# Kernel tuning notes

Measured on AMD Instinct MI355X. Metric: run time of the kernel, lower is better.

Reference implementation:

```python
import jax, jax.numpy as jnp
import numpy as np

D = 1024      # embedding_dim
H = 16        # num_heads
DH = D // H   # head_dim
DFF = 4 * D
EPS = 1e-5


def setup_inputs() -> dict:
    key = jax.random.key(0)
    ks = jax.random.split(key, 10)
    B, T = 2, 2048
    s = 0.02
    return {
        "x": jax.random.normal(ks[0], (B, T, D), dtype=jnp.float32),
        "Wq": jax.random.normal(ks[1], (H, D, DH), dtype=jnp.float32) * s,
        "Wk": jax.random.normal(ks[2], (H, D, DH), dtype=jnp.float32) * s,
        "Wv": jax.random.normal(ks[3], (H, D, DH), dtype=jnp.float32) * s,
        "W1": jax.random.normal(ks[4], (D, DFF), dtype=jnp.float32) * s,
        "b1": jnp.zeros((DFF,), dtype=jnp.float32),
        "W2": jax.random.normal(ks[5], (DFF, D), dtype=jnp.float32) * s,
        "b2": jnp.zeros((D,), dtype=jnp.float32),
        "gamma1": jnp.ones((D,), dtype=jnp.float32),
        "beta1": jnp.zeros((D,), dtype=jnp.float32),
        "gamma2": jnp.ones((D,), dtype=jnp.float32),
        "beta2": jnp.zeros((D,), dtype=jnp.float32),
    }


def _layernorm(x, gamma, beta):
    # torch.var default is unbiased (ddof=1) -- faithful to LayerNorm1d
    mean = jnp.mean(x, axis=-1, keepdims=True)
    var = jnp.var(x, axis=-1, keepdims=True, ddof=1)
    return gamma * (x - mean) * jax.lax.rsqrt(var + EPS) + beta


def _block(x, Wq, Wk, Wv, W1, b1, W2, b2, gamma1, beta1, gamma2, beta2):
    B, T, _ = x.shape
    h = _layernorm(x, gamma1, beta1)
    # per-head projections stacked: [B,H,T,DH]
    Q = jnp.einsum('btd,hde->bhte', h, Wq)
    K = jnp.einsum('btd,hde->bhte', h, Wk)
    V = jnp.einsum('btd,hde->bhte', h, Wv)
    # NOTE: original scales by 1/sqrt(embedding_dim), NOT head_dim
    scores = jnp.einsum('bhqe,bhke->bhqk', Q, K) / jnp.sqrt(jnp.float32(D))
    causal = jnp.tril(jnp.ones((T, T), dtype=bool))
    scores = jnp.where(causal, scores, -jnp.inf)
    attn = jax.nn.softmax(scores, axis=-1)
    out = jnp.einsum('bhqk,bhke->bhqe', attn, V)
    # torch.cat over heads along last dim == transpose+reshape
    out = out.transpose(0, 2, 1, 3).reshape(B, T, D)
    x = x + out
    h2 = _layernorm(x, gamma2, beta2)
    ff = jax.nn.relu(h2 @ W1 + b1) @ W2 + b2  # dropout is identity at inference
    return x + ff


def reference(x, Wq, Wk, Wv, W1, b1, W2, b2, gamma1, beta1, gamma2, beta2):
    return _block(x, Wq, Wk, Wv, W1, b1, W2, b2, gamma1, beta1, gamma2, beta2)
```

## Files before the change

kernel.cpp:

```cpp
#include <hip/hip_runtime.h>

typedef unsigned short u16;
typedef __bf16 bf16;
typedef __attribute__((ext_vector_type(8))) __bf16 bf16x8;
typedef __attribute__((ext_vector_type(4))) float f32x4;
typedef __attribute__((ext_vector_type(8))) unsigned short u16x8;
typedef unsigned long long u64;

__device__ __forceinline__ float bf2f(u16 h) {
  return __uint_as_float(((unsigned int)h) << 16);
}
__device__ __forceinline__ u16 f2bf(float f) {
  unsigned int u = __float_as_uint(f);
  return (u16)((u + 0x7fffu + ((u >> 16) & 1u)) >> 16);
}
__device__ __forceinline__ u16 ld_cv(const void* p, size_t i, int f32) {
  return f32 ? f2bf(((const float*)p)[i]) : ((const u16*)p)[i];
}
__device__ __forceinline__ float ld_f(const void* p, size_t i, int f32) {
  return f32 ? ((const float*)p)[i] : bf2f(((const u16*)p)[i]);
}
__device__ __forceinline__ void async16(const u16* g, u16* l) {
  __builtin_amdgcn_global_load_lds(
      (const __attribute__((address_space(1))) unsigned int*)g,
      (__attribute__((address_space(3))) unsigned int*)l, 16, 0, 0);
}
__device__ __forceinline__ unsigned pk_bf16(float hi, float lo) {
  return __builtin_amdgcn_perm(__float_as_uint(hi) + 0x8000u,
                               __float_as_uint(lo) + 0x8000u, 0x07060302u);
}

__global__ void sniff_kernel(const u16* __restrict__ x, int* __restrict__ flag) {
  const int tid = threadIdx.x;
  int me = 0;
#pragma unroll
  for (int j = 0; j < 4; j++) {
    const u16 v = x[(tid * 4 + j) * 2];
    const int e = (v >> 7) & 0xFF;
    me = me > e ? me : e;
  }
#pragma unroll
  for (int off = 32; off > 0; off >>= 1) {
    const int o = __shfl_down(me, off);
    me = me > o ? me : o;
  }
  __shared__ int sm[4];
  if ((tid & 63) == 0) sm[tid >> 6] = me;
  __syncthreads();
  if (tid == 0) {
    int a = sm[0] > sm[1] ? sm[0] : sm[1];
    int b = sm[2] > sm[3] ? sm[2] : sm[3];
    *flag = ((a > b ? a : b) >= 140) ? 1 : 0;
  }
}

__global__ void prep_kernel(const void* __restrict__ Wq, const void* __restrict__ Wk,
                            const void* __restrict__ Wv, const void* __restrict__ W1,
                            const void* __restrict__ W2,
                            u16* __restrict__ WTq, u16* __restrict__ W1T,
                            u16* __restrict__ W2T, const int* __restrict__ flag) {
  __shared__ u16 tile[64][65];
  const int f = *flag;
  const int bid = blockIdx.x;
  const int lx = threadIdx.x & 63, ly = threadIdx.x >> 6;
  if (bid < 768) {
    const int bx = bid & 15, wh = bid >> 4;
    const int w = wh >> 4, hh = wh & 15;
    const int tr = bx * 64;
    const void* W = (w == 0) ? Wq : ((w == 1) ? Wk : Wv);
    const size_t hbase = (size_t)hh * 65536;
#pragma unroll
    for (int i = 0; i < 16; i++)
      tile[ly * 16 + i][lx] = ld_cv(W, hbase + (size_t)(tr + ly * 16 + i) * 64 + lx, f);
    __syncthreads();
#pragma unroll
    for (int i = 0; i < 16; i++)
      WTq[((size_t)(w * 1024 + hh * 64 + ly * 16 + i)) * 1024 + tr + lx] =
          tile[lx][ly * 16 + i];
  } else {
    const void* src;
    u16* dst;
    int R, C, tc, tr;
    if (bid < 1792) {
      const int j = bid - 768;
      src = W1; dst = W1T; R = 1024; C = 4096;
      tc = (j & 63) * 64; tr = (j >> 6) * 64;
    } else {
      const int j = bid - 1792;
      src = W2; dst = W2T; R = 4096; C = 1024;
      tc = (j & 15) * 64; tr = (j >> 4) * 64;
    }
#pragma unroll
    for (int i = 0; i < 16; i++)
      tile[ly * 16 + i][lx] = ld_cv(src, (size_t)(tr + ly * 16 + i) * C + tc + lx, f);
    __syncthreads();
#pragma unroll
    for (int i = 0; i < 16; i++)
      dst[(size_t)(tc + ly * 16 + i) * R + tr + lx] = tile[lx][ly * 16 + i];
  }
}

template <int EPI, int WR, int WC, bool MS>
__launch_bounds__(WR * WC * 64)
__global__ void gemm_bt(const u16* __restrict__ A, const u16* __restrict__ B,
                        int K, int KLD, int NX, int N,
                        const void* __restrict__ bias, const u16* __restrict__ res,
                        void* __restrict__ out,
                        u16* __restrict__ Qo, u16* __restrict__ Ko, u16* __restrict__ Vto,
                        const int* __restrict__ flag) {
  constexpr int BM = WR * 64, BN = WC * 64, T = WR * WC * 64;
  constexpr int RPA = T / 4;
  constexpr int RAH = BM / RPA;
  constexpr int RBH = BN / RPA;
  __shared__ __align__(16) u16 As[BM * 64];
  __shared__ __align__(16) u16 Bs[BN * 64];
  const int tid = threadIdx.x;
  const int bid = blockIdx.x;
  const int sxp = NX >> 3;
  const int xcd = bid & 7, j9 = bid >> 3;
  int m0, n0, koff = 0, khb = 0;
  if (EPI == 3) {
    m0 = (xcd * 4 + (j9 & 3)) * BM;
    n0 = ((j9 >> 2) & 7) * BN;
    khb = (j9 >> 5) & 1;
    koff = khb * K;
  } else if (MS) {
    m0 = (xcd * sxp + j9 % sxp) * BM;
    n0 = (j9 / sxp) * BN;
  } else {
    n0 = (xcd * sxp + j9 % sxp) * BN;
    m0 = (j9 / sxp) * BM;
  }
  const int wave = tid >> 6, lane = tid & 63;
  const int wm = (wave / WC) * 64, wn = (wave % WC) * 64;
  const int lm = lane & 15, lq = lane >> 4;
  const int fb = (EPI == 1 || EPI == 2) ? *flag : 0;

  const f32x4 zero = {0.f, 0.f, 0.f, 0.f};
  f32x4 acc[4][4];
#pragma unroll
  for (int i = 0; i < 4; i++)
#pragma unroll
    for (int j = 0; j < 4; j++) acc[i][j] = zero;

  const int ar = tid >> 2;
  const int ac = ((tid & 3) ^ ((tid >> 3) & 3)) * 8;
  const u16* Ag = A + (size_t)(m0 + ar) * KLD + koff + ac;
  const u16* Bg = B + (size_t)(n0 + ar) * KLD + koff + ac;
  u16* AsP = &As[tid * 8];
  u16* BsP = &Bs[tid * 8];
  const int rq = (lq ^ ((lm >> 1) & 3)) * 8;

  for (int k0 = 0; k0 < K; k0 += 64) {
#pragma unroll
    for (int hh = 0; hh < 2; hh++) {
#pragma unroll
      for (int c = 0; c < RAH; c++)
        async16(Ag + k0 + hh * 32 + (size_t)c * RPA * KLD,
                AsP + hh * BM * 32 + c * RPA * 32);
#pragma unroll
      for (int c = 0; c < RBH; c++)
        async16(Bg + k0 + hh * 32 + (size_t)c * RPA * KLD,
                BsP + hh * BN * 32 + c * RPA * 32);
    }
    __syncthreads();
    bf16x8 a0[4], a1[4], b0[4], b1[4];
#pragma unroll
    for (int i = 0; i < 4; i++) {
      a0[i] = *(const bf16x8*)&As[(wm + i * 16 + lm) * 32 + rq];
      a1[i] = *(const bf16x8*)&As[BM * 32 + (wm + i * 16 + lm) * 32 + rq];
    }
#pragma unroll
    for (int i = 0; i < 4; i++) {
      b0[i] = *(const bf16x8*)&Bs[(wn + i * 16 + lm) * 32 + rq];
      b1[i] = *(const bf16x8*)&Bs[BN * 32 + (wn + i * 16 + lm) * 32 + rq];
    }
#pragma unroll
    for (int i = 0; i < 4; i++)
#pragma unroll
      for (int j = 0; j < 4; j++) {
        acc[i][j] = __builtin_amdgcn_mfma_f32_16x16x32_bf16(a0[i], b0[j], acc[i][j], 0, 0, 0);
        acc[i][j] = __builtin_amdgcn_mfma_f32_16x16x32_bf16(a1[i], b1[j], acc[i][j], 0, 0, 0);
      }
    __syncthreads();
  }

  if (EPI == 0) {
#pragma unroll
    for (int i = 0; i < 4; i++) {
      const int row0 = m0 + wm + i * 16 + lq * 4;
      const int bb = row0 >> 11, t0 = row0 & 2047;
#pragma unroll
      for (int j = 0; j < 4; j++) {
        const int col = n0 + wn + j * 16 + lm;
        const int w = col >> 10, nn = col & 1023;
        const int hh = nn >> 6, e = nn & 63;
        if (w == 2) {
          ushort4 v4;
          v4.x = f2bf(acc[i][j][0]);
          v4.y = f2bf(acc[i][j][1]);
          v4.z = f2bf(acc[i][j][2]);
          v4.w = f2bf(acc[i][j][3]);
          *(ushort4*)&Vto[(((size_t)(bb * 16 + hh)) * 64 + e) * 2048 + t0] = v4;
        } else {
          u16* dst = (w == 0) ? Qo : Ko;
#pragma unroll
          for (int r = 0; r < 4; r++)
            dst[(((size_t)(bb * 16 + hh)) * 2048 + t0 + r) * 64 + e] =
                f2bf(acc[i][j][r]);
        }
      }
    }
  } else if (EPI == 3) {
    u16* P = khb ? Ko : Qo;
#pragma unroll
    for (int i = 0; i < 4; i++) {
#pragma unroll
      for (int r = 0; r < 4; r++) {
        const int row = m0 + wm + i * 16 + lq * 4 + r;
#pragma unroll
        for (int j = 0; j < 4; j++) {
          const int col = n0 + wn + j * 16 + lm;
          P[(size_t)row * N + col] = f2bf(acc[i][j][r]);
        }
      }
    }
  } else {
#pragma unroll
    for (int i = 0; i < 4; i++) {
#pragma unroll
      for (int r = 0; r < 4; r++) {
        const int row = m0 + wm + i * 16 + lq * 4 + r;
#pragma unroll
        for (int j = 0; j < 4; j++) {
          const int col = n0 + wn + j * 16 + lm;
          const float c = acc[i][j][r];
          if (EPI == 1) {
            const float v = c + ld_f(bias, col, fb);
            ((u16*)out)[(size_t)row * N + col] = f2bf(v > 0.f ? v : 0.f);
          } else {
            const float v = c + ld_f(bias, col, fb) + bf2f(res[(size_t)row * N + col]);
            if (fb)
              ((float*)out)[(size_t)row * N + col] = v;
            else
              ((u16*)out)[(size_t)row * N + col] = f2bf(v);
          }
        }
      }
    }
  }
}

__launch_bounds__(256)
__global__ void ffn2_reduce(const u16* __restrict__ P0, const u16* __restrict__ P1,
                            const void* __restrict__ bias, const u16* __restrict__ res,
                            void* __restrict__ out, const int* __restrict__ flag) {
  const int f = *flag;
  const size_t i0 = ((size_t)blockIdx.x * 256 + threadIdx.x) * 8;
  const int col = (int)(i0 & 1023);
  const u16x8 a8 = *(const u16x8*)(P0 + i0);
  const u16x8 b8 = *(const u16x8*)(P1 + i0);
  const u16x8 r8 = *(const u16x8*)(res + i0);
  float v[8];
#pragma unroll
  for (int k = 0; k < 8; k++)
    v[k] = bf2f(a8[k]) + bf2f(b8[k]) + ld_f(bias, col + k, f) + bf2f(r8[k]);
  if (f) {
    float4 o0 = {v[0], v[1], v[2], v[3]};
    float4 o1 = {v[4], v[5], v[6], v[7]};
    *(float4*)((float*)out + i0) = o0;
    *(float4*)((float*)out + i0 + 4) = o1;
  } else {
    u16x8 o8;
#pragma unroll
    for (int k = 0; k < 8; k++) o8[k] = f2bf(v[k]);
    *(u16x8*)((u16*)out + i0) = o8;
  }
}

__launch_bounds__(256)
__global__ void attn_mfma(const u16* __restrict__ Q, const u16* __restrict__ K,
                          const u16* __restrict__ Vt, const void* __restrict__ xres,
                          const int* __restrict__ flag, u16* __restrict__ x2) {
  __shared__ __align__(16) unsigned char smem[66048];
  const int tid = threadIdx.x;
  const int wave = tid >> 6, lane = tid & 63;
  const int lm = lane & 15, quad = lane >> 4;
  const int bid = blockIdx.x;
  const int xcd = bid & 7, jj = bid >> 3;
  const int bh = xcd + 8 * (jj & 3);
  const int pair = jj >> 2;
  const int b = bh >> 4, h = bh & 15;
  const int f32in = *flag;

  u16* stw = (u16*)smem + wave * 8192;
  float (*Olds)[32][68] = (float(*)[32][68])smem;
  float (*Llds)[2][16] = (float(*)[2][16])(smem + 65536);

  const u16* Kbh = K + (size_t)bh * 131072;
  const u16* Vbh = Vt + (size_t)bh * 131072;
  const f32x4 zero = {0.f, 0.f, 0.f, 0.f};
  const int srow = lane >> 2;
  const int sch2 = ((lane & 3) ^ ((srow >> 1) & 3)) * 8;
  const int rk = (lm >> 1) & 3;

  union V8 { bf16x8 v; struct { u64 lo, hi; } q; };

  auto stageKV = [&](int t, u16* buf) {
    const int ks = t * 32;
#pragma unroll
    for (int hh2 = 0; hh2 < 2; hh2++)
#pragma unroll
      for (int c = 0; c < 2; c++)
        async16(Kbh + (size_t)(ks + c * 16 + srow) * 64 + hh2 * 32 + sch2,
                buf + hh2 * 1024 + c * 512 + lane * 8);
#pragma unroll
    for (int c = 0; c < 4; c++)
      async16(Vbh + (size_t)(c * 16 + srow) * 2048 + ks + sch2,
              buf + 2048 + c * 512 + lane * 8);
  };

#pragma unroll 1
  for (int phase = 0; phase < 2; phase++) {
    const int qb = phase ? (63 - pair) : pair;
    const int qw0 = qb * 32;

    bf16x8 qf[2][2];
#pragma unroll
    for (int s = 0; s < 2; s++) {
      const u16* Qp = Q + ((size_t)bh * 2048 + qw0 + s * 16 + lm) * 64 + quad * 8;
      qf[s][0] = *(const bf16x8*)Qp;
      qf[s][1] = *(const bf16x8*)(Qp + 32);
    }
    f32x4 ot[2][4];
#pragma unroll
    for (int s = 0; s < 2; s++)
#pragma unroll
      for (int j = 0; j < 4; j++) ot[s][j] = zero;
    float l[2] = {0.f, 0.f};

    const int nt = qb + 1;
    const int si = (nt * wave) >> 2;
    const int ei = (nt * (wave + 1)) >> 2;

    if (si < ei) stageKV(si, stw);

#pragma unroll 1
    for (int t = si; t < ei; t++) {
      const u16* Ksw = stw + ((t - si) & 1) * 4096;
      const u16* Vsw = Ksw + 2048;
      if (t + 1 < ei) {
        stageKV(t + 1, stw + ((t - si + 1) & 1) * 4096);
        asm volatile("s_waitcnt vmcnt(8)" ::: "memory");
      } else {
        asm volatile("s_waitcnt vmcnt(0)" ::: "memory");
      }

      f32x4 S[2][2];
      __builtin_amdgcn_s_setprio(1);
#pragma unroll
      for (int s = 0; s < 2; s++)
#pragma unroll
        for (int hh = 0; hh < 2; hh++) {
          const bf16x8 k0 =
              *(const bf16x8*)&Ksw[(hh * 16 + lm) * 32 + (quad ^ rk) * 8];
          const bf16x8 k1 =
              *(const bf16x8*)&Ksw[1024 + (hh * 16 + lm) * 32 + (quad ^ rk) * 8];
          f32x4 a = zero;
          a = __builtin_amdgcn_mfma_f32_16x16x32_bf16(k0, qf[s][0], a, 0, 0, 0);
          a = __builtin_amdgcn_mfma_f32_16x16x32_bf16(k1, qf[s][1], a, 0, 0, 0);
          S[s][hh] = a;
        }
      __builtin_amdgcn_s_setprio(0);

      const bool maskT = (t == qb);
#pragma unroll
      for (int s = 0; s < 2; s++) {
        float p[2][4];
#pragma unroll
        for (int hh = 0; hh < 2; hh++)
#pragma unroll
          for (int r = 0; r < 4; r++)
            p[hh][r] = __expf(S[s][hh][r] * 0.03125f);
        if (maskT) {
#pragma unroll
          for (int hh = 0; hh < 2; hh++)
#pragma unroll
            for (int r = 0; r < 4; r++)
              if (hh * 16 + quad * 4 + r > s * 16 + lm) p[hh][r] = 0.f;
        }
#pragma unroll
        for (int hh = 0; hh < 2; hh++)
#pragma unroll
          for (int r = 0; r < 4; r++) l[s] += p[hh][r];
        unsigned pk[4];
        pk[0] = pk_bf16(p[0][1], p[0][0]);
        pk[1] = pk_bf16(p[0][3], p[0][2]);
        pk[2] = pk_bf16(p[1][1], p[1][0]);
        pk[3] = pk_bf16(p[1][3], p[1][2]);
        const bf16x8 pf = *(const bf16x8*)pk;
        __builtin_amdgcn_s_setprio(1);
#pragma unroll
        for (int j = 0; j < 4; j++) {
          V8 vf;
          vf.q.lo = *(const u64*)&Vsw[(j * 16 + lm) * 32 +
                                      (((quad >> 1)) ^ rk) * 8 + (quad & 1) * 4];
          vf.q.hi = *(const u64*)&Vsw[(j * 16 + lm) * 32 +
                                      (((quad >> 1) | 2) ^ rk) * 8 + (quad & 1) * 4];
          ot[s][j] = __builtin_amdgcn_mfma_f32_16x16x32_bf16(vf.v, pf, ot[s][j], 0, 0, 0);
        }
        __builtin_amdgcn_s_setprio(0);
      }
    }

#pragma unroll
    for (int s = 0; s < 2; s++) {
      l[s] += __shfl_xor(l[s], 16);
      l[s] += __shfl_xor(l[s], 32);
    }

    __syncthreads();

#pragma unroll
    for (int s = 0; s < 2; s++)
#pragma unroll
      for (int j = 0; j < 4; j++)
        *(f32x4*)&Olds[wave][s * 16 + lm][j * 16 + quad * 4] = ot[s][j];
    if (quad == 0) {
      Llds[wave][0][lm] = l[0];
      Llds[wave][1][lm] = l[1];
    }
    __syncthreads();
    const int q = tid >> 3;
    const int e0 = (tid & 7) * 8;
    f32x4 oa = zero, ob = zero;
#pragma unroll
    for (int w = 0; w < 4; w++) {
      oa += *(const f32x4*)&Olds[w][q][e0];
      ob += *(const f32x4*)&Olds[w][q][e0 + 4];
    }
    const float lt = Llds[0][q >> 4][q & 15] + Llds[1][q >> 4][q & 15] +
                     Llds[2][q >> 4][q & 15] + Llds[3][q >> 4][q & 15];
    const float linv = 1.f / lt;
    const size_t rowbase = ((size_t)(b * 2048 + qw0 + q)) * 1024 + h * 64 + e0;
    float xv[8];
    if (f32in) {
      const float* xf = (const float*)xres + rowbase;
      const float4 u0 = *(const float4*)xf;
      const float4 u1 = *(const float4*)(xf + 4);
      xv[0] = u0.x; xv[1] = u0.y; xv[2] = u0.z; xv[3] = u0.w;
      xv[4] = u1.x; xv[5] = u1.y; xv[6] = u1.z; xv[7] = u1.w;
    } else {
      const u16x8 u = *(const u16x8*)((const u16*)xres + rowbase);
#pragma unroll
      for (int k = 0; k < 8; k++) xv[k] = bf2f(u[k]);
    }
    u16x8 o8;
#pragma unroll
    for (int k = 0; k < 4; k++) o8[k] = f2bf(xv[k] + oa[k] * linv);
#pragma unroll
    for (int k = 0; k < 4; k++) o8[4 + k] = f2bf(xv[4 + k] + ob[k] * linv);
    *(u16x8*)&x2[rowbase] = o8;
    __syncthreads();
  }
}

__launch_bounds__(256)
__global__ void ln_kernel(const void* __restrict__ x, const void* __restrict__ gamma,
                          const void* __restrict__ beta, u16* __restrict__ out,
                          const int* __restrict__ flag, int xraw) {
  const size_t row = blockIdx.x;
  const int tid = threadIdx.x;
  const int f = *flag;
  const int fx = xraw ? f : 0;
  float v0, v1, v2, v3;
  if (fx) {
    const float4 v = *((const float4*)x + row * 256 + tid);
    v0 = v.x; v1 = v.y; v2 = v.z; v3 = v.w;
  } else {
    const ushort4 u = *((const ushort4*)x + row * 256 + tid);
    v0 = bf2f(u.x); v1 = bf2f(u.y); v2 = bf2f(u.z); v3 = bf2f(u.w);
  }
  float s = v0 + v1 + v2 + v3;
  float sq = v0 * v0 + v1 * v1 + v2 * v2 + v3 * v3;
#pragma unroll
  for (int off = 32; off > 0; off >>= 1) {
    s += __shfl_down(s, off);
    sq += __shfl_down(sq, off);
  }
  __shared__ float ss[4], ssq[4];
  if ((tid & 63) == 0) { ss[tid >> 6] = s; ssq[tid >> 6] = sq; }
  __syncthreads();
  s = ss[0] + ss[1] + ss[2] + ss[3];
  sq = ssq[0] + ssq[1] + ssq[2] + ssq[3];
  const float mean = s * (1.f / 1024.f);
  const float var = (sq - 1024.f * mean * mean) * (1.f / 1023.f);
  const float rs = rsqrtf(var + 1e-5f);
  const int c0 = tid * 4;
  ushort4 o;
  o.x = f2bf(ld_f(gamma, c0 + 0, f) * (v0 - mean) * rs + ld_f(beta, c0 + 0, f));
  o.y = f2bf(ld_f(gamma, c0 + 1, f) * (v1 - mean) * rs + ld_f(beta, c0 + 1, f));
  o.z = f2bf(ld_f(gamma, c0 + 2, f) * (v2 - mean) * rs + ld_f(beta, c0 + 2, f));
  o.w = f2bf(ld_f(gamma, c0 + 3, f) * (v3 - mean) * rs + ld_f(beta, c0 + 3, f));
  *(ushort4*)&out[row * 1024 + tid * 4] = o;
}

extern "C" void kernel_launch(void* const* d_in, const int* in_sizes, int n_in,
                              void* d_out, int out_size, void* d_ws, size_t ws_size,
                              hipStream_t stream) {
  const void* x      = d_in[0];
  const void* Wq     = d_in[1];
  const void* Wk     = d_in[2];
  const void* Wv     = d_in[3];
  const void* W1     = d_in[4];
  const void* b1     = d_in[5];
  const void* W2     = d_in[6];
  const void* b2     = d_in[7];
  const void* gamma1 = d_in[8];
  const void* beta1  = d_in[9];
  const void* gamma2 = d_in[10];
  const void* beta2  = d_in[11];
  u16* ws = (u16*)d_ws;

  const size_t M4 = 4194304;
  u16* h   = ws;
  u16* Qb  = ws + 1 * M4;
  u16* Kb  = ws + 2 * M4;
  u16* Vtb = ws + 3 * M4;
  u16* WTq = ws + 4 * M4;
  u16* x2  = ws + 4 * M4;
  u16* h2  = ws + 5 * M4;
  u16* W1T = ws + 6 * M4;
  u16* W2T = ws + 7 * M4;
  u16* ff1 = ws;
  u16* P0  = ws + 5 * M4;
  u16* P1  = ws + 6 * M4;
  int* flag = (int*)(ws + 8 * M4 + 9216);

  sniff_kernel<<<1, 256, 0, stream>>>((const u16*)x, flag);
  prep_kernel<<<2816, 256, 0, stream>>>(Wq, Wk, Wv, W1, W2, WTq, W1T, W2T, flag);
  ln_kernel<<<4096, 256, 0, stream>>>(x, gamma1, beta1, h, flag, 1);
  gemm_bt<0, 4, 2, false><<<384, 512, 0, stream>>>(h, WTq, 1024, 1024, 24, 3072,
                                                   nullptr, nullptr, nullptr,
                                                   Qb, Kb, Vtb, flag);
  attn_mfma<<<1024, 256, 0, stream>>>(Qb, Kb, Vtb, x, flag, x2);
  ln_kernel<<<4096, 256, 0, stream>>>(x2, gamma2, beta2, h2, flag, 0);
  gemm_bt<1, 4, 2, false><<<512, 512, 0, stream>>>(h2, W1T, 1024, 1024, 32, 4096,
                                                   b1, nullptr, ff1,
                                                   nullptr, nullptr, nullptr, flag);
  gemm_bt<3, 2, 2, false><<<512, 256, 0, stream>>>(ff1, W2T, 2048, 4096, 8, 1024,
                                                   nullptr, nullptr, nullptr,
                                                   P0, P1, nullptr, flag);
  ffn2_reduce<<<2048, 256, 0, stream>>>(P0, P1, b2, x2, d_out, flag);
}
```

Measured before the change: 325.2 us.

## Restructure attention so each wave owns a query block sharing cooperatively staged K/V

The attention kernel switches from splitting the KV range of one query block across four waves (with an LDS reduction of partial outputs and row sums) to giving each wave its own 32-row query block. Two early and two late blocks share one block so causal work balances. K/V tiles are staged cooperatively by all waves into a shared double buffer with barriers, and LDS shrinks from about 66 KB to 16 KB with launch bounds allowing two blocks per CU. This removes the cross-wave reduction and the phase loop but adds per-tile block barriers and idle waves once their causal range ends. The grid is halved to 512 blocks.

```diff
diff --git a/kernel.cpp b/kernel.cpp
--- a/kernel.cpp
+++ b/kernel.cpp
@@ -278,24 +278,22 @@
   }
 }
 
-__launch_bounds__(256)
+__launch_bounds__(256, 2)
 __global__ void attn_mfma(const u16* __restrict__ Q, const u16* __restrict__ K,
                           const u16* __restrict__ Vt, const void* __restrict__ xres,
                           const int* __restrict__ flag, u16* __restrict__ x2) {
-  __shared__ __align__(16) unsigned char smem[66048];
+  __shared__ __align__(16) u16 smem[2][4096];
   const int tid = threadIdx.x;
   const int wave = tid >> 6, lane = tid & 63;
   const int lm = lane & 15, quad = lane >> 4;
   const int bid = blockIdx.x;
-  const int xcd = bid & 7, jj = bid >> 3;
-  const int bh = xcd + 8 * (jj & 3);
-  const int pair = jj >> 2;
+  const int bh = (bid & 7) + 8 * ((bid >> 3) & 3);
+  const int p = bid >> 5;
   const int b = bh >> 4, h = bh & 15;
   const int f32in = *flag;
-
-  u16* stw = (u16*)smem + wave * 8192;
-  float (*Olds)[32][68] = (float(*)[32][68])smem;
-  float (*Llds)[2][16] = (float(*)[2][16])(smem + 65536);
+  const int qb = (wave < 2) ? (2 * p + wave) : (63 - 2 * p - (wave & 1));
+  const int qw0 = qb * 32;
+  const int nt = 64 - 2 * p;
 
   const u16* Kbh = K + (size_t)bh * 131072;
   const u16* Vbh = Vt + (size_t)bh * 131072;
@@ -304,164 +302,136 @@
   const int sch2 = ((lane & 3) ^ ((srow >> 1) & 3)) * 8;
   const int rk = (lm >> 1) & 3;
 
+  bf16x8 qf[2][2];
+#pragma unroll
+  for (int s = 0; s < 2; s++) {
+    const u16* Qp = Q + ((size_t)bh * 2048 + qw0 + s * 16 + lm) * 64 + quad * 8;
+    qf[s][0] = *(const bf16x8*)Qp;
+    qf[s][1] = *(const bf16x8*)(Qp + 32);
+  }
+  __builtin_amdgcn_s_waitcnt(0x0F70);
+
+  f32x4 ot[2][4];
+#pragma unroll
+  for (int s = 0; s < 2; s++)
+#pragma unroll
+    for (int j = 0; j < 4; j++) ot[s][j] = zero;
+  float l[2] = {0.f, 0.f};
+
   union V8 { bf16x8 v; struct { u64 lo, hi; } q; };
 
-  auto stageKV = [&](int t, u16* buf) {
+  auto stage2 = [&](int t, u16* buf) {
     const int ks = t * 32;
-#pragma unroll
-    for (int hh2 = 0; hh2 < 2; hh2++)
+    if (wave < 2) {
 #pragma unroll
       for (int c = 0; c < 2; c++)
-        async16(Kbh + (size_t)(ks + c * 16 + srow) * 64 + hh2 * 32 + sch2,
-                buf + hh2 * 1024 + c * 512 + lane * 8);
-#pragma unroll
-    for (int c = 0; c < 4; c++)
-      async16(Vbh + (size_t)(c * 16 + srow) * 2048 + ks + sch2,
-              buf + 2048 + c * 512 + lane * 8);
+        async16(Kbh + (size_t)(ks + c * 16 + srow) * 64 + wave * 32 + sch2,
+                buf + wave * 1024 + c * 512 + lane * 8);
+    } else {
+      const int cb = (wave & 1) * 2;
+#pragma unroll
+      for (int c = cb; c < cb + 2; c++)
+        async16(Vbh + (size_t)(c * 16 + srow) * 2048 + ks + sch2,
+                buf + 2048 + c * 512 + lane * 8);
+    }
   };
 
+  stage2(0, smem[0]);
+
 #pragma unroll 1
-  for (int phase = 0; phase < 2; phase++) {
-    const int qb = phase ? (63 - pair) : pair;
-    const int qw0 = qb * 32;
-
-    bf16x8 qf[2][2];
-#pragma unroll
-    for (int s = 0; s < 2; s++) {
-      const u16* Qp = Q + ((size_t)bh * 2048 + qw0 + s * 16 + lm) * 64 + quad * 8;
-      qf[s][0] = *(const bf16x8*)Qp;
-      qf[s][1] = *(const bf16x8*)(Qp + 32);
-    }
-    f32x4 ot[2][4];
-#pragma unroll
-    for (int s = 0; s < 2; s++)
-#pragma unroll
-      for (int j = 0; j < 4; j++) ot[s][j] = zero;
-    float l[2] = {0.f, 0.f};
-
-    const int nt = qb + 1;
-    const int si = (nt * wave) >> 2;
-    const int ei = (nt * (wave + 1)) >> 2;
-
-    if (si < ei) stageKV(si, stw);
-
-#pragma unroll 1
-    for (int t = si; t < ei; t++) {
-      const u16* Ksw = stw + ((t - si) & 1) * 4096;
+  for (int t = 0; t < nt; t++) {
+    if (t + 1 < nt) {
+      stage2(t + 1, smem[(t + 1) & 1]);
+      asm volatile("s_waitcnt vmcnt(2)" ::: "memory");
+    } else {
+      asm volatile("s_waitcnt vmcnt(0)" ::: "memory");
+    }
+    __builtin_amdgcn_s_barrier();
+    if (t <= qb) {
+      const u16* Ksw = smem[t & 1];
       const u16* Vsw = Ksw + 2048;
-      if (t + 1 < ei) {
-        stageKV(t + 1, stw + ((t - si + 1) & 1) * 4096);
-        asm volatile("s_waitcnt vmcnt(8)" ::: "memory");
-      } else {
-        asm volatile("s_waitcnt vmcnt(0)" ::: "memory");
-      }
-
+      bf16x8 kk[2][2];
+#pragma unroll
+      for (int hh = 0; hh < 2; hh++) {
+        kk[hh][0] = *(const bf16x8*)&Ksw[(hh * 16 + lm) * 32 + (quad ^ rk) * 8];
+        kk[hh][1] = *(const bf16x8*)&Ksw[1024 + (hh * 16 + lm) * 32 + (quad ^ rk) * 8];
+      }
+      V8 vf[4];
+#pragma unroll
+      for (int j = 0; j < 4; j++) {
+        vf[j].q.lo = *(const u64*)&Vsw[(j * 16 + lm) * 32 +
+                                       (((quad >> 1)) ^ rk) * 8 + (quad & 1) * 4];
+        vf[j].q.hi = *(const u64*)&Vsw[(j * 16 + lm) * 32 +
+                                       (((quad >> 1) | 2) ^ rk) * 8 + (quad & 1) * 4];
+      }
       f32x4 S[2][2];
       __builtin_amdgcn_s_setprio(1);
 #pragma unroll
       for (int s = 0; s < 2; s++)
 #pragma unroll
         for (int hh = 0; hh < 2; hh++) {
-          const bf16x8 k0 =
-              *(const bf16x8*)&Ksw[(hh * 16 + lm) * 32 + (quad ^ rk) * 8];
-          const bf16x8 k1 =
-              *(const bf16x8*)&Ksw[1024 + (hh * 16 + lm) * 32 + (quad ^ rk) * 8];
           f32x4 a = zero;
-          a = __builtin_amdgcn_mfma_f32_16x16x32_bf16(k0, qf[s][0], a, 0, 0, 0);
-          a = __builtin_amdgcn_mfma_f32_16x16x32_bf16(k1, qf[s][1], a, 0, 0, 0);
+          a = __builtin_amdgcn_mfma_f32_16x16x32_bf16(kk[hh][0], qf[s][0], a, 0, 0, 0);
+          a = __builtin_amdgcn_mfma_f32_16x16x32_bf16(kk[hh][1], qf[s][1], a, 0, 0, 0);
           S[s][hh] = a;
         }
       __builtin_amdgcn_s_setprio(0);
-
       const bool maskT = (t == qb);
 #pragma unroll
       for (int s = 0; s < 2; s++) {
-        float p[2][4];
+        float pv[2][4];
 #pragma unroll
         for (int hh = 0; hh < 2; hh++)
 #pragma unroll
-          for (int r = 0; r < 4; r++)
-            p[hh][r] = __expf(S[s][hh][r] * 0.03125f);
-        if (maskT) {
-#pragma unroll
-          for (int hh = 0; hh < 2; hh++)
-#pragma unroll
-            for (int r = 0; r < 4; r++)
-              if (hh * 16 + quad * 4 + r > s * 16 + lm) p[hh][r] = 0.f;
-        }
-#pragma unroll
-        for (int hh = 0; hh < 2; hh++)
-#pragma unroll
-          for (int r = 0; r < 4; r++) l[s] += p[hh][r];
+          for (int r = 0; r < 4; r++) {
+            float v = __expf(S[s][hh][r] * 0.03125f);
+            if (maskT && (hh * 16 + quad * 4 + r > s * 16 + lm)) v = 0.f;
+            l[s] += v;
+            pv[hh][r] = v;
+          }
         unsigned pk[4];
-        pk[0] = pk_bf16(p[0][1], p[0][0]);
-        pk[1] = pk_bf16(p[0][3], p[0][2]);
-        pk[2] = pk_bf16(p[1][1], p[1][0]);
-        pk[3] = pk_bf16(p[1][3], p[1][2]);
+        pk[0] = pk_bf16(pv[0][1], pv[0][0]);
+        pk[1] = pk_bf16(pv[0][3], pv[0][2]);
+        pk[2] = pk_bf16(pv[1][1], pv[1][0]);
+        pk[3] = pk_bf16(pv[1][3], pv[1][2]);
         const bf16x8 pf = *(const bf16x8*)pk;
         __builtin_amdgcn_s_setprio(1);
 #pragma unroll
-        for (int j = 0; j < 4; j++) {
-          V8 vf;
-          vf.q.lo = *(const u64*)&Vsw[(j * 16 + lm) * 32 +
-                                      (((quad >> 1)) ^ rk) * 8 + (quad & 1) * 4];
-          vf.q.hi = *(const u64*)&Vsw[(j * 16 + lm) * 32 +
-                                      (((quad >> 1) | 2) ^ rk) * 8 + (quad & 1) * 4];
-          ot[s][j] = __builtin_amdgcn_mfma_f32_16x16x32_bf16(vf.v, pf, ot[s][j], 0, 0, 0);
-        }
+        for (int j = 0; j < 4; j++)
+          ot[s][j] = __builtin_amdgcn_mfma_f32_16x16x32_bf16(vf[j].v, pf, ot[s][j], 0, 0, 0);
         __builtin_amdgcn_s_setprio(0);
       }
     }
-
-#pragma unroll
-    for (int s = 0; s < 2; s++) {
-      l[s] += __shfl_xor(l[s], 16);
-      l[s] += __shfl_xor(l[s], 32);
-    }
-
-    __syncthreads();
-
-#pragma unroll
-    for (int s = 0; s < 2; s++)
-#pragma unroll
-      for (int j = 0; j < 4; j++)
-        *(f32x4*)&Olds[wave][s * 16 + lm][j * 16 + quad * 4] = ot[s][j];
-    if (quad == 0) {
-      Llds[wave][0][lm] = l[0];
-      Llds[wave][1][lm] = l[1];
-    }
-    __syncthreads();
-    const int q = tid >> 3;
-    const int e0 = (tid & 7) * 8;
-    f32x4 oa = zero, ob = zero;
-#pragma unroll
-    for (int w = 0; w < 4; w++) {
-      oa += *(const f32x4*)&Olds[w][q][e0];
-      ob += *(const f32x4*)&Olds[w][q][e0 + 4];
-    }
-    const float lt = Llds[0][q >> 4][q & 15] + Llds[1][q >> 4][q & 15] +
-                     Llds[2][q >> 4][q & 15] + Llds[3][q >> 4][q & 15];
-    const float linv = 1.f / lt;
-    const size_t rowbase = ((size_t)(b * 2048 + qw0 + q)) * 1024 + h * 64 + e0;
-    float xv[8];
-    if (f32in) {
-      const float* xf = (const float*)xres + rowbase;
-      const float4 u0 = *(const float4*)xf;
-      const float4 u1 = *(const float4*)(xf + 4);
-      xv[0] = u0.x; xv[1] = u0.y; xv[2] = u0.z; xv[3] = u0.w;
-      xv[4] = u1.x; xv[5] = u1.y; xv[6] = u1.z; xv[7] = u1.w;
-    } else {
-      const u16x8 u = *(const u16x8*)((const u16*)xres + rowbase);
-#pragma unroll
-      for (int k = 0; k < 8; k++) xv[k] = bf2f(u[k]);
-    }
-    u16x8 o8;
-#pragma unroll
-    for (int k = 0; k < 4; k++) o8[k] = f2bf(xv[k] + oa[k] * linv);
-#pragma unroll
-    for (int k = 0; k < 4; k++) o8[4 + k] = f2bf(xv[4 + k] + ob[k] * linv);
-    *(u16x8*)&x2[rowbase] = o8;
-    __syncthreads();
+    __builtin_amdgcn_s_barrier();
+  }
+
+#pragma unroll
+  for (int s = 0; s < 2; s++) {
+    l[s] += __shfl_xor(l[s], 16);
+    l[s] += __shfl_xor(l[s], 32);
+  }
+#pragma unroll
+  for (int s = 0; s < 2; s++) {
+    const float linv = 1.f / l[s];
+    const int row = qw0 + s * 16 + lm;
+    const size_t rb = ((size_t)(b * 2048 + row)) * 1024 + h * 64 + quad * 4;
+#pragma unroll
+    for (int j = 0; j < 4; j++) {
+      float xv[4];
+      if (f32in) {
+        const float4 u = *(const float4*)((const float*)xres + rb + j * 16);
+        xv[0] = u.x; xv[1] = u.y; xv[2] = u.z; xv[3] = u.w;
+      } else {
+        const ushort4 u = *(const ushort4*)((const u16*)xres + rb + j * 16);
+        xv[0] = bf2f(u.x); xv[1] = bf2f(u.y); xv[2] = bf2f(u.z); xv[3] = bf2f(u.w);
+      }
+      ushort4 o;
+      o.x = f2bf(xv[0] + ot[s][j][0] * linv);
+      o.y = f2bf(xv[1] + ot[s][j][1] * linv);
+      o.z = f2bf(xv[2] + ot[s][j][2] * linv);
+      o.w = f2bf(xv[3] + ot[s][j][3] * linv);
+      *(ushort4*)&x2[rb + j * 16] = o;
+    }
   }
 }
 
@@ -543,7 +513,7 @@
   gemm_bt<0, 4, 2, false><<<384, 512, 0, stream>>>(h, WTq, 1024, 1024, 24, 3072,
                                                    nullptr, nullptr, nullptr,
                                                    Qb, Kb, Vtb, flag);
-  attn_mfma<<<1024, 256, 0, stream>>>(Qb, Kb, Vtb, x, flag, x2);
+  attn_mfma<<<512, 256, 0, stream>>>(Qb, Kb, Vtb, x, flag, x2);
   ln_kernel<<<4096, 256, 0, stream>>>(x2, gamma2, beta2, h2, flag, 0);
   gemm_bt<1, 4, 2, false><<<512, 512, 0, stream>>>(h2, W1T, 1024, 1024, 32, 4096,
                                                    b1, nullptr, ff1,
```

Measured after the change: 324.5 us. About the same (-0.2%).
